# Performance work log

Hardware: AMD Instinct MI355X
Metric: run time of the kernel (lower is better)

Reference implementation:

```python
import math
import jax, jax.numpy as jnp
import numpy as np
from jax import lax

# Fractional-order LIF constants (Teka et al. style fractional LIF)
ALPHA = 0.2          # fractional order (self.frac_order)
DT = 0.1             # ms
V_L = -70.0          # leak reversal
V_RESET = -70.0      # reset potential
V_TH = -50.0         # spike threshold
G_L = 0.025          # leak conductance
CM = 0.5             # membrane capacitance
KAPPA = (DT ** ALPHA) * math.gamma(2.0 - ALPHA)
EXPO = 1.0 - ALPHA


def _flif_scan(I_seq):
    """Fractional LIF over time. I_seq: [T, B, H] -> (spikes, mems) each [T, B, H].
    V_n = KAPPA * (-G_L*(V_{n-1}-V_L) + I_n)/CM + V_{n-1} - memory_n,
    memory_n = sum_{j=1}^{n-1} c_j * dV_{n-1-j},  c_j = (j+1)^{1-a} - j^{1-a}."""
    T, B, H = I_seq.shape
    dt_f = I_seq.dtype
    j = jnp.arange(T + 1, dtype=jnp.float32)
    c = ((j + 1.0) ** EXPO - j ** EXPO).astype(dt_f)  # c[j], valid for j>=1
    ks = jnp.arange(T)

    def step(carry, xs):
        V, hist = carry            # V: [B,H], hist[k] = dV_k: [T,B,H]
        I, n = xs                  # n = 1..T (1-based step index)
        jidx = n - 1 - ks          # lag j for each history slot k
        w = jnp.where(jidx >= 1, c[jnp.clip(jidx, 0, T)], 0.0)
        memory = jnp.einsum('t,tbh->bh', w, hist)
        f = (-G_L * (V - V_L) + I) / CM
        Vn = KAPPA * f + V - memory
        spk = (Vn >= V_TH).astype(dt_f)
        Vr = jnp.where(spk > 0, V_RESET, Vn)
        hist = hist.at[n - 1].set(Vr - V)
        return (Vr, hist), (spk, Vr)

    V0 = jnp.full((B, H), V_RESET, dtype=dt_f)
    hist0 = jnp.zeros((T, B, H), dtype=dt_f)
    _, (spikes, mems) = lax.scan(step, (V0, hist0), (I_seq, jnp.arange(1, T + 1)))
    return spikes, mems


def setup_inputs() -> dict:
    key = jax.random.key(0)
    k1, k2, k3 = jax.random.split(key, 3)
    B, T, NI, NH, NO = 64, 128, 784, 512, 10
    data = jax.random.uniform(k1, (B, T, NI), dtype=jnp.float32)
    kh = 1.0 / np.sqrt(NI)
    W_h = jnp.abs(jax.random.uniform(k2, (NH, NI), minval=-kh, maxval=kh, dtype=jnp.float32) * 6.0)
    ko = 1.0 / np.sqrt(NH)
    W_o = jnp.abs(jax.random.uniform(k3, (NO, NH), minval=-ko, maxval=ko, dtype=jnp.float32) * 5.0)
    return {"data": data, "W_h": W_h, "W_o": W_o}


def reference(data, W_h, W_o):
    # hidden synapses: [B,T,NI] x [NH,NI] -> [T,B,NH] (time-major for scan)
    I_h = jnp.einsum('btn,hn->tbh', data, W_h)
    spk_h, mem_h = _flif_scan(I_h)
    # output synapses applied per step == one GEMM over all steps
    I_o = jnp.einsum('tbh,oh->tbo', spk_h, W_o)
    spk_o, mem_o = _flif_scan(I_o)
    # matches torch.stack(output_spikes_trace), torch.stack(output_values_trace): [T,B,NO]
    return spk_o, mem_o
```

## Files before the change

### kernel.cpp

```cpp
#include <hip/hip_runtime.h>
#include <hip/hip_bf16.h>
#include <cmath>

#define T_STEPS 128
#define BATCH   64
#define NI      784
#define NIP     800
#define NH      512
#define NO      10
#define M1      (T_STEPS*BATCH)
#define NT_H    (BATCH*NH)
#define NT_O    (BATCH*NO)
#define OUT_HALF (T_STEPS*BATCH*NO)
#define TB      8

typedef __attribute__((ext_vector_type(8))) short short8;
typedef __attribute__((ext_vector_type(4))) float f32x4;
typedef __attribute__((ext_vector_type(8))) unsigned short u16x8;

static __device__ __forceinline__ unsigned short f2b_bits(float x) {
    __hip_bfloat16 h = __float2bfloat16(x);
    return *reinterpret_cast<unsigned short*>(&h);
}
static __device__ __forceinline__ float b2f_bits(unsigned short u) {
    union { unsigned int i; float f; } v; v.i = ((unsigned int)u) << 16; return v.f;
}

__global__ __launch_bounds__(256) void prep_kernel(const float* __restrict__ data,
                                                   const float* __restrict__ Wh,
                                                   __hip_bfloat16* __restrict__ Ab,
                                                   __hip_bfloat16* __restrict__ Whb,
                                                   float* __restrict__ ctab) {
    const int bid = blockIdx.x;
    if (bid == 0) {
        const int j = threadIdx.x;
        if (j < 192) {
            double a = pow((double)(j + 1), 0.8);
            double b = pow((double)j, 0.8);
            ctab[j] = (float)(a - b);
        }
        return;
    }
    if (bid <= 6400) {
        const int idx = (bid - 1) * 256 + threadIdx.x;
        const int r  = idx / 200;
        const int n4 = (idx - r * 200) * 4;
        const int t = r >> 6, b = r & 63;
        const int srow = b * T_STEPS + t;
        ushort4 o;
        if (n4 < NI) {
            const float4 f = *reinterpret_cast<const float4*>(data + (size_t)srow * NI + n4);
            o.x = f2b_bits(f.x); o.y = f2b_bits(f.y); o.z = f2b_bits(f.z); o.w = f2b_bits(f.w);
        } else {
            o.x = o.y = o.z = o.w = 0;
        }
        *reinterpret_cast<ushort4*>(Ab + (size_t)r * NIP + n4) = o;
    } else {
        const int idx = (bid - 6401) * 256 + threadIdx.x;
        const int r  = idx / 200;
        const int n4 = (idx - r * 200) * 4;
        ushort4 o;
        if (n4 < NI) {
            const float4 f = *reinterpret_cast<const float4*>(Wh + (size_t)r * NI + n4);
            o.x = f2b_bits(f.x); o.y = f2b_bits(f.y); o.z = f2b_bits(f.z); o.w = f2b_bits(f.w);
        } else {
            o.x = o.y = o.z = o.w = 0;
        }
        *reinterpret_cast<ushort4*>(Whb + (size_t)r * NIP + n4) = o;
    }
}

__global__ __launch_bounds__(256) void gemm_bf16_kernel(const __hip_bfloat16* __restrict__ A,
                                                        const __hip_bfloat16* __restrict__ B,
                                                        __hip_bfloat16* __restrict__ C,
                                                        int N, int Kp) {
    __shared__ __hip_bfloat16 As[2][128 * 32];
    __shared__ __hip_bfloat16 Bs[2][128 * 32];
    const int tid  = threadIdx.x;
    const int wave = tid >> 6, lane = tid & 63;
    const int wm = wave >> 1, wn = wave & 1;
    const int bm = blockIdx.x, bn = blockIdx.y;
    const int lrow = lane >> 2;
    const int lchk = lane & 3;

    const int NTILES = Kp / 32;

    auto STAGE = [&](int buf, int tt) {
        const int k0 = tt * 32;
#pragma unroll
        for (int p = 0; p < 2; ++p) {
            const int rbase = p * 64 + wave * 16;
            {
                const __hip_bfloat16* g = A + (size_t)(bm * 128 + rbase + lrow) * Kp + k0 + lchk * 8;
                __builtin_amdgcn_global_load_lds((const __attribute__((address_space(1))) void*)g,
                                                 (__attribute__((address_space(3))) void*)(As[buf] + rbase * 32),
                                                 16, 0, 0);
            }
            {
                const __hip_bfloat16* g = B + (size_t)(bn * 128 + rbase + lrow) * Kp + k0 + lchk * 8;
                __builtin_amdgcn_global_load_lds((const __attribute__((address_space(1))) void*)g,
                                                 (__attribute__((address_space(3))) void*)(Bs[buf] + rbase * 32),
                                                 16, 0, 0);
            }
        }
    };

    f32x4 acc[4][4] = {};

    STAGE(0, 0);
    __syncthreads();

    int cur = 0;
    for (int t = 0; t < NTILES; ++t) {
        if (t + 1 < NTILES) STAGE(cur ^ 1, t + 1);

        short8 a[4], b[4];
#pragma unroll
        for (int i = 0; i < 4; ++i)
            a[i] = *reinterpret_cast<const short8*>(As[cur] + (wm * 64 + i * 16 + (lane & 15)) * 32 + (lane >> 4) * 8);
#pragma unroll
        for (int j = 0; j < 4; ++j)
            b[j] = *reinterpret_cast<const short8*>(Bs[cur] + (wn * 64 + j * 16 + (lane & 15)) * 32 + (lane >> 4) * 8);
#pragma unroll
        for (int i = 0; i < 4; ++i)
#pragma unroll
            for (int j = 0; j < 4; ++j)
                acc[i][j] = __builtin_amdgcn_mfma_f32_16x16x32_bf16(a[i], b[j], acc[i][j], 0, 0, 0);

        __syncthreads();
        cur ^= 1;
    }

#pragma unroll
    for (int i = 0; i < 4; ++i) {
#pragma unroll
        for (int j = 0; j < 4; ++j) {
            const int col = bn * 128 + wn * 64 + j * 16 + (lane & 15);
#pragma unroll
            for (int r2 = 0; r2 < 4; ++r2) {
                const int row = bm * 128 + wm * 64 + i * 16 + (lane >> 4) * 4 + r2;
                C[(size_t)row * N + col] = __float2bfloat16(acc[i][j][r2]);
            }
        }
    }
}

template <bool FINAL>
__global__ __launch_bounds__(64) void flif_scan_kernel(const void* __restrict__ Iin,
                                                       void* __restrict__ spikes,
                                                       float* __restrict__ mems,
                                                       const float* __restrict__ ctab,
                                                       int NT, float kappa) {
    __shared__ float hist[T_STEPS * 64];
    __shared__ __attribute__((aligned(16))) float cs[192];
    __shared__ __attribute__((aligned(16))) char inps[FINAL ? T_STEPS * 64 * 4 : T_STEPS * 64 * 2];
    const int lane = threadIdx.x;
    const int nid  = blockIdx.x * 64 + lane;

    if constexpr (!FINAL) {
#pragma unroll
        for (int q = 0; q < 16; ++q) {
            const __hip_bfloat16* g = (const __hip_bfloat16*)Iin +
                ((size_t)(q * 8 + (lane >> 3)) * NT + (size_t)blockIdx.x * 64 + (lane & 7) * 8);
            __builtin_amdgcn_global_load_lds((const __attribute__((address_space(1))) void*)g,
                                             (__attribute__((address_space(3))) void*)(inps + q * 1024),
                                             16, 0, 0);
        }
    } else {
#pragma unroll
        for (int q = 0; q < 32; ++q) {
            const float* g = (const float*)Iin +
                ((size_t)(q * 4 + (lane >> 4)) * NT + (size_t)blockIdx.x * 64 + (lane & 15) * 4);
            __builtin_amdgcn_global_load_lds((const __attribute__((address_space(1))) void*)g,
                                             (__attribute__((address_space(3))) void*)(inps + q * 1024),
                                             16, 0, 0);
        }
    }

    for (int j = lane; j < 192; j += 64) cs[j] = ctab[j];
    __syncthreads();

    float cn_[TB];
#pragma unroll
    for (int j = 0; j < TB; ++j) cn_[j] = cs[j];

    float V = -70.f;
    unsigned dvbits = 0u;

    for (int t = 0; t < T_STEPS / TB; ++t) {
        const int n0 = t * TB;

        float Ivv[TB];
#pragma unroll
        for (int i = 0; i < TB; ++i) {
            if constexpr (FINAL) Ivv[i] = ((const float*)inps)[(n0 + i) * 64 + lane];
            else                 Ivv[i] = __bfloat162float(((const __hip_bfloat16*)inps)[(n0 + i) * 64 + lane]);
        }
        __builtin_amdgcn_sched_barrier(0);

        float old_[TB];
#pragma unroll
        for (int i = 0; i < TB; ++i) old_[i] = 0.f;

        if (__any(dvbits != 0u)) {
            for (int k0 = 0; k0 < n0; k0 += TB) {
                float hv[TB];
                unsigned sb = 0u;
#pragma unroll
                for (int kk = 0; kk < TB; ++kk) {
                    hv[kk] = hist[(k0 + kk) * 64 + lane];
                    sb |= __float_as_uint(hv[kk]);
                }
                if (__any(sb != 0u)) {
                    const int base = n0 - k0 - (TB - 1);
                    float cw[2 * TB];
#pragma unroll
                    for (int q = 0; q < 4; ++q) {
                        const float4 cv = *reinterpret_cast<const float4*>(cs + (base - 1) + 4 * q);
                        cw[4 * q + 0] = cv.x; cw[4 * q + 1] = cv.y;
                        cw[4 * q + 2] = cv.z; cw[4 * q + 3] = cv.w;
                    }
#pragma unroll
                    for (int kk = 0; kk < TB; ++kk) {
#pragma unroll
                        for (int i = 0; i < TB; ++i)
                            old_[i] += hv[kk] * cw[TB - kk + i];
                    }
                }
            }
        }

        float dvb[TB];
#pragma unroll
        for (int i = 0; i < TB; ++i) {
            const int nm1 = n0 + i;
            const float Iv = Ivv[i];
            const float f  = (-0.025f * (V + 70.f) + Iv) * 2.0f;
            const float Vn = kappa * f + V - old_[i];
            const bool  sp = (Vn >= -50.f);
            const float Vr = sp ? -70.f : Vn;
            const float dv = Vr - V;
            dvb[i] = dv;
            dvbits |= __float_as_uint(dv);
#pragma unroll
            for (int i2 = i + 1; i2 < TB; ++i2)
                old_[i2] += dv * cn_[i2 - i];
            if (FINAL) {
                ((float*)spikes)[(size_t)nm1 * NT + nid] = sp ? 1.f : 0.f;
                mems[(size_t)nm1 * NT + nid] = Vr;
            } else {
                ((__hip_bfloat16*)spikes)[(size_t)nm1 * NT + nid] = __float2bfloat16(sp ? 1.f : 0.f);
            }
            V = Vr;
        }

        __builtin_amdgcn_sched_barrier(0);
#pragma unroll
        for (int i = 0; i < TB; ++i)
            hist[(n0 + i) * 64 + lane] = dvb[i];
        __builtin_amdgcn_sched_barrier(0);
    }
}

__global__ __launch_bounds__(256) void gemm2_kernel(const __hip_bfloat16* __restrict__ S,
                                                    const float* __restrict__ Wo,
                                                    float* __restrict__ Io) {
    const int wave = threadIdx.x >> 6, lane = threadIdx.x & 63;
    const int r0 = (blockIdx.x * 4 + wave) * 4;

    float wreg[NO][8];
#pragma unroll
    for (int o = 0; o < NO; ++o) {
        const float4 w0 = *reinterpret_cast<const float4*>(Wo + (size_t)o * NH + lane * 8);
        const float4 w1 = *reinterpret_cast<const float4*>(Wo + (size_t)o * NH + lane * 8 + 4);
        wreg[o][0] = w0.x; wreg[o][1] = w0.y; wreg[o][2] = w0.z; wreg[o][3] = w0.w;
        wreg[o][4] = w1.x; wreg[o][5] = w1.y; wreg[o][6] = w1.z; wreg[o][7] = w1.w;
    }

#pragma unroll
    for (int rr = 0; rr < 4; ++rr) {
        const int r = r0 + rr;
        u16x8 raw = *reinterpret_cast<const u16x8*>(S + (size_t)r * NH + lane * 8);
        float s[8];
#pragma unroll
        for (int j = 0; j < 8; ++j) s[j] = b2f_bits(raw[j]);
#pragma unroll
        for (int o = 0; o < NO; ++o) {
            float a = 0.f;
#pragma unroll
            for (int j = 0; j < 8; ++j) a += s[j] * wreg[o][j];
#pragma unroll
            for (int off = 32; off; off >>= 1) a += __shfl_xor(a, off);
            if (lane == o) Io[(size_t)r * NO + o] = a;
        }
    }
}

extern "C" void kernel_launch(void* const* d_in, const int* in_sizes, int n_in,
                              void* d_out, int out_size, void* d_ws, size_t ws_size,
                              hipStream_t stream) {
    const float* data = (const float*)d_in[0];
    const float* Wh   = (const float*)d_in[1];
    const float* Wo   = (const float*)d_in[2];
    float* out = (float*)d_out;

    char* ws = (char*)d_ws;
    size_t off = 0;
    auto alloc = [&](size_t bytes) { void* p = ws + off; off += (bytes + 255) & ~255ull; return p; };
    __hip_bfloat16* Ab   = (__hip_bfloat16*)alloc((size_t)M1 * NIP * 2);
    __hip_bfloat16* Whb  = (__hip_bfloat16*)alloc((size_t)NH * NIP * 2);
    __hip_bfloat16* Ih   = (__hip_bfloat16*)alloc((size_t)M1 * NH * 2);
    __hip_bfloat16* Sh   = (__hip_bfloat16*)alloc((size_t)M1 * NH * 2);
    float*          Io   = (float*)alloc((size_t)M1 * NO * 4);
    float*          ctab = (float*)alloc(192 * 4);

    const float kappa = (float)(std::pow(0.1, 0.2) * std::tgamma(1.8));

    prep_kernel<<<6801, 256, 0, stream>>>(data, Wh, Ab, Whb, ctab);

    dim3 g1(M1 / 128, NH / 128, 1);
    gemm_bf16_kernel<<<g1, 256, 0, stream>>>(Ab, Whb, Ih, NH, NIP);

    flif_scan_kernel<false><<<NT_H / 64, 64, 0, stream>>>(Ih, Sh, nullptr, ctab, NT_H, kappa);

    gemm2_kernel<<<M1 / 16, 256, 0, stream>>>(Sh, Wo, Io);

    flif_scan_kernel<true><<<NT_O / 64, 64, 0, stream>>>(Io, out, out + OUT_HALF, ctab, NT_O, kappa);
}
```

Before: 69.50 us.

## Fuse bf16 conversion, hidden GEMM and hidden LIF scan into one kernel

Replaces the separate prep, bf16 GEMM and hidden-layer scan kernels with one fused kernel. Each block loads fp32 input and weight tiles, converts them to bf16 in registers, computes a 128x128 time-by-neuron tile with MFMA, keeps the currents in LDS and runs the fractional LIF scan there. This removes the bf16 staging buffers and the round trip of the hidden currents through global memory, and drops two launches. The decay coefficient table is now built on the host and copied in. In exchange, each block uses 128KB of LDS, which limits occupancy. The GEMM uses register prefetch instead of async LDS double buffering, and the input data is re-read once per hidden-column block.

```diff
diff --git a/kernel.cpp b/kernel.cpp
--- a/kernel.cpp
+++ b/kernel.cpp
@@ -26,160 +26,13 @@
     union { unsigned int i; float f; } v; v.i = ((unsigned int)u) << 16; return v.f;
 }
 
-__global__ __launch_bounds__(256) void prep_kernel(const float* __restrict__ data,
-                                                   const float* __restrict__ Wh,
-                                                   __hip_bfloat16* __restrict__ Ab,
-                                                   __hip_bfloat16* __restrict__ Whb,
-                                                   float* __restrict__ ctab) {
-    const int bid = blockIdx.x;
-    if (bid == 0) {
-        const int j = threadIdx.x;
-        if (j < 192) {
-            double a = pow((double)(j + 1), 0.8);
-            double b = pow((double)j, 0.8);
-            ctab[j] = (float)(a - b);
-        }
-        return;
-    }
-    if (bid <= 6400) {
-        const int idx = (bid - 1) * 256 + threadIdx.x;
-        const int r  = idx / 200;
-        const int n4 = (idx - r * 200) * 4;
-        const int t = r >> 6, b = r & 63;
-        const int srow = b * T_STEPS + t;
-        ushort4 o;
-        if (n4 < NI) {
-            const float4 f = *reinterpret_cast<const float4*>(data + (size_t)srow * NI + n4);
-            o.x = f2b_bits(f.x); o.y = f2b_bits(f.y); o.z = f2b_bits(f.z); o.w = f2b_bits(f.w);
-        } else {
-            o.x = o.y = o.z = o.w = 0;
-        }
-        *reinterpret_cast<ushort4*>(Ab + (size_t)r * NIP + n4) = o;
-    } else {
-        const int idx = (bid - 6401) * 256 + threadIdx.x;
-        const int r  = idx / 200;
-        const int n4 = (idx - r * 200) * 4;
-        ushort4 o;
-        if (n4 < NI) {
-            const float4 f = *reinterpret_cast<const float4*>(Wh + (size_t)r * NI + n4);
-            o.x = f2b_bits(f.x); o.y = f2b_bits(f.y); o.z = f2b_bits(f.z); o.w = f2b_bits(f.w);
-        } else {
-            o.x = o.y = o.z = o.w = 0;
-        }
-        *reinterpret_cast<ushort4*>(Whb + (size_t)r * NIP + n4) = o;
-    }
-}
-
-__global__ __launch_bounds__(256) void gemm_bf16_kernel(const __hip_bfloat16* __restrict__ A,
-                                                        const __hip_bfloat16* __restrict__ B,
-                                                        __hip_bfloat16* __restrict__ C,
-                                                        int N, int Kp) {
-    __shared__ __hip_bfloat16 As[2][128 * 32];
-    __shared__ __hip_bfloat16 Bs[2][128 * 32];
-    const int tid  = threadIdx.x;
-    const int wave = tid >> 6, lane = tid & 63;
-    const int wm = wave >> 1, wn = wave & 1;
-    const int bm = blockIdx.x, bn = blockIdx.y;
-    const int lrow = lane >> 2;
-    const int lchk = lane & 3;
-
-    const int NTILES = Kp / 32;
-
-    auto STAGE = [&](int buf, int tt) {
-        const int k0 = tt * 32;
-#pragma unroll
-        for (int p = 0; p < 2; ++p) {
-            const int rbase = p * 64 + wave * 16;
-            {
-                const __hip_bfloat16* g = A + (size_t)(bm * 128 + rbase + lrow) * Kp + k0 + lchk * 8;
-                __builtin_amdgcn_global_load_lds((const __attribute__((address_space(1))) void*)g,
-                                                 (__attribute__((address_space(3))) void*)(As[buf] + rbase * 32),
-                                                 16, 0, 0);
-            }
-            {
-                const __hip_bfloat16* g = B + (size_t)(bn * 128 + rbase + lrow) * Kp + k0 + lchk * 8;
-                __builtin_amdgcn_global_load_lds((const __attribute__((address_space(1))) void*)g,
-                                                 (__attribute__((address_space(3))) void*)(Bs[buf] + rbase * 32),
-                                                 16, 0, 0);
-            }
-        }
-    };
-
-    f32x4 acc[4][4] = {};
-
-    STAGE(0, 0);
-    __syncthreads();
-
-    int cur = 0;
-    for (int t = 0; t < NTILES; ++t) {
-        if (t + 1 < NTILES) STAGE(cur ^ 1, t + 1);
-
-        short8 a[4], b[4];
-#pragma unroll
-        for (int i = 0; i < 4; ++i)
-            a[i] = *reinterpret_cast<const short8*>(As[cur] + (wm * 64 + i * 16 + (lane & 15)) * 32 + (lane >> 4) * 8);
-#pragma unroll
-        for (int j = 0; j < 4; ++j)
-            b[j] = *reinterpret_cast<const short8*>(Bs[cur] + (wn * 64 + j * 16 + (lane & 15)) * 32 + (lane >> 4) * 8);
-#pragma unroll
-        for (int i = 0; i < 4; ++i)
-#pragma unroll
-            for (int j = 0; j < 4; ++j)
-                acc[i][j] = __builtin_amdgcn_mfma_f32_16x16x32_bf16(a[i], b[j], acc[i][j], 0, 0, 0);
-
-        __syncthreads();
-        cur ^= 1;
-    }
-
-#pragma unroll
-    for (int i = 0; i < 4; ++i) {
-#pragma unroll
-        for (int j = 0; j < 4; ++j) {
-            const int col = bn * 128 + wn * 64 + j * 16 + (lane & 15);
-#pragma unroll
-            for (int r2 = 0; r2 < 4; ++r2) {
-                const int row = bm * 128 + wm * 64 + i * 16 + (lane >> 4) * 4 + r2;
-                C[(size_t)row * N + col] = __float2bfloat16(acc[i][j][r2]);
-            }
-        }
-    }
-}
-
-template <bool FINAL>
-__global__ __launch_bounds__(64) void flif_scan_kernel(const void* __restrict__ Iin,
-                                                       void* __restrict__ spikes,
-                                                       float* __restrict__ mems,
-                                                       const float* __restrict__ ctab,
-                                                       int NT, float kappa) {
-    __shared__ float hist[T_STEPS * 64];
-    __shared__ __attribute__((aligned(16))) float cs[192];
-    __shared__ __attribute__((aligned(16))) char inps[FINAL ? T_STEPS * 64 * 4 : T_STEPS * 64 * 2];
-    const int lane = threadIdx.x;
-    const int nid  = blockIdx.x * 64 + lane;
-
-    if constexpr (!FINAL) {
-#pragma unroll
-        for (int q = 0; q < 16; ++q) {
-            const __hip_bfloat16* g = (const __hip_bfloat16*)Iin +
-                ((size_t)(q * 8 + (lane >> 3)) * NT + (size_t)blockIdx.x * 64 + (lane & 7) * 8);
-            __builtin_amdgcn_global_load_lds((const __attribute__((address_space(1))) void*)g,
-                                             (__attribute__((address_space(3))) void*)(inps + q * 1024),
-                                             16, 0, 0);
-        }
-    } else {
-#pragma unroll
-        for (int q = 0; q < 32; ++q) {
-            const float* g = (const float*)Iin +
-                ((size_t)(q * 4 + (lane >> 4)) * NT + (size_t)blockIdx.x * 64 + (lane & 15) * 4);
-            __builtin_amdgcn_global_load_lds((const __attribute__((address_space(1))) void*)g,
-                                             (__attribute__((address_space(3))) void*)(inps + q * 1024),
-                                             16, 0, 0);
-        }
-    }
-
-    for (int j = lane; j < 192; j += 64) cs[j] = ctab[j];
-    __syncthreads();
-
+template <bool FINAL, int STRIDE>
+__device__ __forceinline__ void flif_scan_body(const char* __restrict__ inps,
+                                               float* __restrict__ hist,
+                                               const float* __restrict__ cs,
+                                               void* __restrict__ spikes,
+                                               float* __restrict__ mems,
+                                               int NT, int nid, int li, float kappa) {
     float cn_[TB];
 #pragma unroll
     for (int j = 0; j < TB; ++j) cn_[j] = cs[j];
@@ -193,8 +46,8 @@
         float Ivv[TB];
 #pragma unroll
         for (int i = 0; i < TB; ++i) {
-            if constexpr (FINAL) Ivv[i] = ((const float*)inps)[(n0 + i) * 64 + lane];
-            else                 Ivv[i] = __bfloat162float(((const __hip_bfloat16*)inps)[(n0 + i) * 64 + lane]);
+            if constexpr (FINAL) Ivv[i] = ((const float*)inps)[(n0 + i) * STRIDE + li];
+            else                 Ivv[i] = __bfloat162float(((const __hip_bfloat16*)inps)[(n0 + i) * STRIDE + li]);
         }
         __builtin_amdgcn_sched_barrier(0);
 
@@ -208,7 +61,7 @@
                 unsigned sb = 0u;
 #pragma unroll
                 for (int kk = 0; kk < TB; ++kk) {
-                    hv[kk] = hist[(k0 + kk) * 64 + lane];
+                    hv[kk] = hist[(k0 + kk) * STRIDE + li];
                     sb |= __float_as_uint(hv[kk]);
                 }
                 if (__any(sb != 0u)) {
@@ -257,8 +110,116 @@
         __builtin_amdgcn_sched_barrier(0);
 #pragma unroll
         for (int i = 0; i < TB; ++i)
-            hist[(n0 + i) * 64 + lane] = dvb[i];
+            hist[(n0 + i) * STRIDE + li] = dvb[i];
         __builtin_amdgcn_sched_barrier(0);
+    }
+}
+
+__global__ __launch_bounds__(256) void fused1_kernel(const float* __restrict__ data,
+                                                     const float* __restrict__ Wh,
+                                                     __hip_bfloat16* __restrict__ Sh,
+                                                     const float* __restrict__ ctab,
+                                                     float kappa) {
+    __shared__ __attribute__((aligned(16))) char SMEM[131072];
+    __hip_bfloat16* As   = (__hip_bfloat16*)SMEM;
+    __hip_bfloat16* Bs   = (__hip_bfloat16*)(SMEM + 16384);
+    __hip_bfloat16* Ibuf = (__hip_bfloat16*)(SMEM + 32768);
+    float*          hist = (float*)(SMEM + 65536);
+    float*          cs   = (float*)SMEM;
+
+    const int tid  = threadIdx.x;
+    const int wave = tid >> 6, lane = tid & 63;
+    const int wm = wave >> 1, wn = wave & 1;
+    const int b  = blockIdx.x;
+    const int hn = blockIdx.y;
+
+    const int NTILES = NIP / 32;
+
+    float4 ra[4], rb[4];
+    auto LOADT = [&](int t) {
+        const int k0 = t * 32;
+#pragma unroll
+        for (int q = 0; q < 4; ++q) {
+            const int idx = tid + 256 * q;
+            const int row = idx >> 3;
+            const int c4  = idx & 7;
+            const int gk  = k0 + c4 * 4;
+            if (gk < NI) {
+                ra[q] = *reinterpret_cast<const float4*>(data + (size_t)(b * 128 + row) * NI + gk);
+                rb[q] = *reinterpret_cast<const float4*>(Wh   + (size_t)(hn * 128 + row) * NI + gk);
+            } else {
+                ra[q] = make_float4(0.f, 0.f, 0.f, 0.f);
+                rb[q] = make_float4(0.f, 0.f, 0.f, 0.f);
+            }
+        }
+    };
+    auto WRITET = [&]() {
+#pragma unroll
+        for (int q = 0; q < 4; ++q) {
+            const int idx = tid + 256 * q;
+            const int row = idx >> 3;
+            const int c4  = idx & 7;
+            ushort4 oa, ob;
+            oa.x = f2b_bits(ra[q].x); oa.y = f2b_bits(ra[q].y);
+            oa.z = f2b_bits(ra[q].z); oa.w = f2b_bits(ra[q].w);
+            ob.x = f2b_bits(rb[q].x); ob.y = f2b_bits(rb[q].y);
+            ob.z = f2b_bits(rb[q].z); ob.w = f2b_bits(rb[q].w);
+            *reinterpret_cast<ushort4*>(As + row * 32 + c4 * 4) = oa;
+            *reinterpret_cast<ushort4*>(Bs + row * 32 + c4 * 4) = ob;
+        }
+    };
+
+    f32x4 acc[4][4] = {};
+
+    LOADT(0);
+    WRITET();
+    __syncthreads();
+
+    for (int t = 0; t < NTILES; ++t) {
+        if (t + 1 < NTILES) LOADT(t + 1);
+        __builtin_amdgcn_sched_barrier(0);
+
+        short8 a[4], bfr[4];
+#pragma unroll
+        for (int i = 0; i < 4; ++i)
+            a[i] = *reinterpret_cast<const short8*>(As + (wm * 64 + i * 16 + (lane & 15)) * 32 + (lane >> 4) * 8);
+#pragma unroll
+        for (int j = 0; j < 4; ++j)
+            bfr[j] = *reinterpret_cast<const short8*>(Bs + (wn * 64 + j * 16 + (lane & 15)) * 32 + (lane >> 4) * 8);
+#pragma unroll
+        for (int i = 0; i < 4; ++i)
+#pragma unroll
+            for (int j = 0; j < 4; ++j)
+                acc[i][j] = __builtin_amdgcn_mfma_f32_16x16x32_bf16(a[i], bfr[j], acc[i][j], 0, 0, 0);
+
+        __syncthreads();
+        if (t + 1 < NTILES) {
+            WRITET();
+            __syncthreads();
+        }
+    }
+
+#pragma unroll
+    for (int i = 0; i < 4; ++i) {
+#pragma unroll
+        for (int j = 0; j < 4; ++j) {
+            const int col = wn * 64 + j * 16 + (lane & 15);
+#pragma unroll
+            for (int r2 = 0; r2 < 4; ++r2) {
+                const int row = wm * 64 + i * 16 + (lane >> 4) * 4 + r2;
+                Ibuf[row * 128 + col] = __float2bfloat16(acc[i][j][r2]);
+            }
+        }
+    }
+    __syncthreads();
+
+    for (int j = tid; j < 192; j += 256) cs[j] = ctab[j];
+    __syncthreads();
+
+    if (tid < 128) {
+        flif_scan_body<false, 128>((const char*)Ibuf, hist, cs,
+                                   (void*)(Sh + (size_t)b * NH), nullptr,
+                                   64 * NH, hn * 128 + tid, tid, kappa);
     }
 }
 
@@ -294,6 +255,31 @@
             if (lane == o) Io[(size_t)r * NO + o] = a;
         }
     }
+}
+
+__global__ __launch_bounds__(64) void flif_final_kernel(const float* __restrict__ Io,
+                                                        float* __restrict__ spikes,
+                                                        float* __restrict__ mems,
+                                                        const float* __restrict__ ctab,
+                                                        float kappa) {
+    __shared__ float hist[T_STEPS * 64];
+    __shared__ __attribute__((aligned(16))) float cs[192];
+    __shared__ __attribute__((aligned(16))) char inps[T_STEPS * 64 * 4];
+    const int lane = threadIdx.x;
+    const int nid  = blockIdx.x * 64 + lane;
+
+#pragma unroll
+    for (int q = 0; q < 32; ++q) {
+        const float* g = Io +
+            ((size_t)(q * 4 + (lane >> 4)) * NT_O + (size_t)blockIdx.x * 64 + (lane & 15) * 4);
+        __builtin_amdgcn_global_load_lds((const __attribute__((address_space(1))) void*)g,
+                                         (__attribute__((address_space(3))) void*)(inps + q * 1024),
+                                         16, 0, 0);
+    }
+    for (int j = lane; j < 192; j += 64) cs[j] = ctab[j];
+    __syncthreads();
+
+    flif_scan_body<true, 64>(inps, hist, cs, spikes, mems, NT_O, nid, lane, kappa);
 }
 
 extern "C" void kernel_launch(void* const* d_in, const int* in_sizes, int n_in,
@@ -307,23 +293,21 @@
     char* ws = (char*)d_ws;
     size_t off = 0;
     auto alloc = [&](size_t bytes) { void* p = ws + off; off += (bytes + 255) & ~255ull; return p; };
-    __hip_bfloat16* Ab   = (__hip_bfloat16*)alloc((size_t)M1 * NIP * 2);
-    __hip_bfloat16* Whb  = (__hip_bfloat16*)alloc((size_t)NH * NIP * 2);
-    __hip_bfloat16* Ih   = (__hip_bfloat16*)alloc((size_t)M1 * NH * 2);
     __hip_bfloat16* Sh   = (__hip_bfloat16*)alloc((size_t)M1 * NH * 2);
     float*          Io   = (float*)alloc((size_t)M1 * NO * 4);
     float*          ctab = (float*)alloc(192 * 4);
 
     const float kappa = (float)(std::pow(0.1, 0.2) * std::tgamma(1.8));
 
-    prep_kernel<<<6801, 256, 0, stream>>>(data, Wh, Ab, Whb, ctab);
-
-    dim3 g1(M1 / 128, NH / 128, 1);
-    gemm_bf16_kernel<<<g1, 256, 0, stream>>>(Ab, Whb, Ih, NH, NIP);
-
-    flif_scan_kernel<false><<<NT_H / 64, 64, 0, stream>>>(Ih, Sh, nullptr, ctab, NT_H, kappa);
+    static float h_ctab[192];
+    for (int j = 0; j < 192; ++j)
+        h_ctab[j] = (float)(std::pow((double)(j + 1), 0.8) - std::pow((double)j, 0.8));
+    hipMemcpyAsync(ctab, h_ctab, 192 * sizeof(float), hipMemcpyHostToDevice, stream);
+
+    dim3 g1(BATCH, NH / 128, 1);
+    fused1_kernel<<<g1, 256, 0, stream>>>(data, Wh, Sh, ctab, kappa);
 
     gemm2_kernel<<<M1 / 16, 256, 0, stream>>>(Sh, Wo, Io);
 
-    flif_scan_kernel<true><<<NT_O / 64, 64, 0, stream>>>(Io, out, out + OUT_HALF, ctab, NT_O, kappa);
-}
+    flif_final_kernel<<<NT_O / 64, 64, 0, stream>>>(Io, out, out + OUT_HALF, ctab, kappa);
+}
```

New measurement: 94.22 us. 35.6% more time.

## Fuse hidden-layer GEMM with the fractional LIF scan per batch tile

Applied to the files above, without the earlier changes.

Merges the first bf16 MFMA GEMM and the hidden-layer fractional LIF scan into one kernel. Each block computes a 128-timestep by 64-neuron tile for a single batch element, keeps the currents in shared memory, and then runs the scan on one wave. This removes the global round trip of the hidden currents and one kernel launch. In exchange, the GEMM tile shrinks (64 wide in N), shared-memory use per block rises, and only one of four waves does the serial scan while the others sit idle.

```diff
diff --git a/kernel.cpp b/kernel.cpp
--- a/kernel.cpp
+++ b/kernel.cpp
@@ -24,6 +24,95 @@
 }
 static __device__ __forceinline__ float b2f_bits(unsigned short u) {
     union { unsigned int i; float f; } v; v.i = ((unsigned int)u) << 16; return v.f;
+}
+
+template <bool FINAL, int STRIDE>
+__device__ __forceinline__ void flif_scan_body(const char* __restrict__ inps,
+                                               float* __restrict__ hist,
+                                               const float* __restrict__ cs,
+                                               void* __restrict__ spikes,
+                                               float* __restrict__ mems,
+                                               int NT, int nid, int li, float kappa) {
+    float cn_[TB];
+#pragma unroll
+    for (int j = 0; j < TB; ++j) cn_[j] = cs[j];
+
+    float V = -70.f;
+    unsigned dvbits = 0u;
+
+    for (int t = 0; t < T_STEPS / TB; ++t) {
+        const int n0 = t * TB;
+
+        float Ivv[TB];
+#pragma unroll
+        for (int i = 0; i < TB; ++i) {
+            if constexpr (FINAL) Ivv[i] = ((const float*)inps)[(n0 + i) * STRIDE + li];
+            else                 Ivv[i] = __bfloat162float(((const __hip_bfloat16*)inps)[(n0 + i) * STRIDE + li]);
+        }
+        __builtin_amdgcn_sched_barrier(0);
+
+        float old_[TB];
+#pragma unroll
+        for (int i = 0; i < TB; ++i) old_[i] = 0.f;
+
+        if (__any(dvbits != 0u)) {
+            for (int k0 = 0; k0 < n0; k0 += TB) {
+                float hv[TB];
+                unsigned sb = 0u;
+#pragma unroll
+                for (int kk = 0; kk < TB; ++kk) {
+                    hv[kk] = hist[(k0 + kk) * STRIDE + li];
+                    sb |= __float_as_uint(hv[kk]);
+                }
+                if (__any(sb != 0u)) {
+                    const int base = n0 - k0 - (TB - 1);
+                    float cw[2 * TB];
+#pragma unroll
+                    for (int q = 0; q < 4; ++q) {
+                        const float4 cv = *reinterpret_cast<const float4*>(cs + (base - 1) + 4 * q);
+                        cw[4 * q + 0] = cv.x; cw[4 * q + 1] = cv.y;
+                        cw[4 * q + 2] = cv.z; cw[4 * q + 3] = cv.w;
+                    }
+#pragma unroll
+                    for (int kk = 0; kk < TB; ++kk) {
+#pragma unroll
+                        for (int i = 0; i < TB; ++i)
+                            old_[i] += hv[kk] * cw[TB - kk + i];
+                    }
+                }
+            }
+        }
+
+        float dvb[TB];
+#pragma unroll
+        for (int i = 0; i < TB; ++i) {
+            const int nm1 = n0 + i;
+            const float Iv = Ivv[i];
+            const float f  = (-0.025f * (V + 70.f) + Iv) * 2.0f;
+            const float Vn = kappa * f + V - old_[i];
+            const bool  sp = (Vn >= -50.f);
+            const float Vr = sp ? -70.f : Vn;
+            const float dv = Vr - V;
+            dvb[i] = dv;
+            dvbits |= __float_as_uint(dv);
+#pragma unroll
+            for (int i2 = i + 1; i2 < TB; ++i2)
+                old_[i2] += dv * cn_[i2 - i];
+            if (FINAL) {
+                ((float*)spikes)[(size_t)nm1 * NT + nid] = sp ? 1.f : 0.f;
+                mems[(size_t)nm1 * NT + nid] = Vr;
+            } else {
+                ((__hip_bfloat16*)spikes)[(size_t)nm1 * NT + nid] = __float2bfloat16(sp ? 1.f : 0.f);
+            }
+            V = Vr;
+        }
+
+        __builtin_amdgcn_sched_barrier(0);
+#pragma unroll
+        for (int i = 0; i < TB; ++i)
+            hist[(n0 + i) * STRIDE + li] = dvb[i];
+        __builtin_amdgcn_sched_barrier(0);
+    }
 }
 
 __global__ __launch_bounds__(256) void prep_kernel(const float* __restrict__ data,
@@ -70,42 +159,46 @@
     }
 }
 
-__global__ __launch_bounds__(256) void gemm_bf16_kernel(const __hip_bfloat16* __restrict__ A,
-                                                        const __hip_bfloat16* __restrict__ B,
-                                                        __hip_bfloat16* __restrict__ C,
-                                                        int N, int Kp) {
+__global__ __launch_bounds__(256) void fused1_kernel(const __hip_bfloat16* __restrict__ A,
+                                                     const __hip_bfloat16* __restrict__ B,
+                                                     __hip_bfloat16* __restrict__ Sh,
+                                                     const float* __restrict__ ctab,
+                                                     float kappa) {
     __shared__ __hip_bfloat16 As[2][128 * 32];
-    __shared__ __hip_bfloat16 Bs[2][128 * 32];
+    __shared__ __hip_bfloat16 Bs[2][64 * 32];
+    __shared__ __hip_bfloat16 Ibuf[128 * 64];
+    __shared__ float          hist[128 * 64];
+    __shared__ __attribute__((aligned(16))) float cs[192];
+
     const int tid  = threadIdx.x;
     const int wave = tid >> 6, lane = tid & 63;
     const int wm = wave >> 1, wn = wave & 1;
-    const int bm = blockIdx.x, bn = blockIdx.y;
+    const int b  = blockIdx.x;
+    const int hn = blockIdx.y;
     const int lrow = lane >> 2;
     const int lchk = lane & 3;
 
-    const int NTILES = Kp / 32;
+    const int NTILES = NIP / 32;
 
     auto STAGE = [&](int buf, int tt) {
         const int k0 = tt * 32;
 #pragma unroll
         for (int p = 0; p < 2; ++p) {
             const int rbase = p * 64 + wave * 16;
-            {
-                const __hip_bfloat16* g = A + (size_t)(bm * 128 + rbase + lrow) * Kp + k0 + lchk * 8;
-                __builtin_amdgcn_global_load_lds((const __attribute__((address_space(1))) void*)g,
-                                                 (__attribute__((address_space(3))) void*)(As[buf] + rbase * 32),
-                                                 16, 0, 0);
-            }
-            {
-                const __hip_bfloat16* g = B + (size_t)(bn * 128 + rbase + lrow) * Kp + k0 + lchk * 8;
-                __builtin_amdgcn_global_load_lds((const __attribute__((address_space(1))) void*)g,
-                                                 (__attribute__((address_space(3))) void*)(Bs[buf] + rbase * 32),
-                                                 16, 0, 0);
-            }
+            const __hip_bfloat16* g = A + (size_t)((rbase + lrow) * 64 + b) * NIP + k0 + lchk * 8;
+            __builtin_amdgcn_global_load_lds((const __attribute__((address_space(1))) void*)g,
+                                             (__attribute__((address_space(3))) void*)(As[buf] + rbase * 32),
+                                             16, 0, 0);
+        }
+        {
+            const __hip_bfloat16* g = B + (size_t)(hn * 64 + wave * 16 + lrow) * NIP + k0 + lchk * 8;
+            __builtin_amdgcn_global_load_lds((const __attribute__((address_space(1))) void*)g,
+                                             (__attribute__((address_space(3))) void*)(Bs[buf] + wave * 16 * 32),
+                                             16, 0, 0);
         }
     };
 
-    f32x4 acc[4][4] = {};
+    f32x4 acc[4][2] = {};
 
     STAGE(0, 0);
     __syncthreads();
@@ -114,18 +207,18 @@
     for (int t = 0; t < NTILES; ++t) {
         if (t + 1 < NTILES) STAGE(cur ^ 1, t + 1);
 
-        short8 a[4], b[4];
+        short8 a[4], bb[2];
 #pragma unroll
         for (int i = 0; i < 4; ++i)
             a[i] = *reinterpret_cast<const short8*>(As[cur] + (wm * 64 + i * 16 + (lane & 15)) * 32 + (lane >> 4) * 8);
 #pragma unroll
-        for (int j = 0; j < 4; ++j)
-            b[j] = *reinterpret_cast<const short8*>(Bs[cur] + (wn * 64 + j * 16 + (lane & 15)) * 32 + (lane >> 4) * 8);
+        for (int j = 0; j < 2; ++j)
+            bb[j] = *reinterpret_cast<const short8*>(Bs[cur] + (wn * 32 + j * 16 + (lane & 15)) * 32 + (lane >> 4) * 8);
 #pragma unroll
         for (int i = 0; i < 4; ++i)
 #pragma unroll
-            for (int j = 0; j < 4; ++j)
-                acc[i][j] = __builtin_amdgcn_mfma_f32_16x16x32_bf16(a[i], b[j], acc[i][j], 0, 0, 0);
+            for (int j = 0; j < 2; ++j)
+                acc[i][j] = __builtin_amdgcn_mfma_f32_16x16x32_bf16(a[i], bb[j], acc[i][j], 0, 0, 0);
 
         __syncthreads();
         cur ^= 1;
@@ -134,131 +227,24 @@
 #pragma unroll
     for (int i = 0; i < 4; ++i) {
 #pragma unroll
-        for (int j = 0; j < 4; ++j) {
-            const int col = bn * 128 + wn * 64 + j * 16 + (lane & 15);
+        for (int j = 0; j < 2; ++j) {
+            const int col = wn * 32 + j * 16 + (lane & 15);
 #pragma unroll
             for (int r2 = 0; r2 < 4; ++r2) {
-                const int row = bm * 128 + wm * 64 + i * 16 + (lane >> 4) * 4 + r2;
-                C[(size_t)row * N + col] = __float2bfloat16(acc[i][j][r2]);
+                const int row = wm * 64 + i * 16 + (lane >> 4) * 4 + r2;
+                Ibuf[row * 64 + col] = __float2bfloat16(acc[i][j][r2]);
             }
         }
     }
-}
-
-template <bool FINAL>
-__global__ __launch_bounds__(64) void flif_scan_kernel(const void* __restrict__ Iin,
-                                                       void* __restrict__ spikes,
-                                                       float* __restrict__ mems,
-                                                       const float* __restrict__ ctab,
-                                                       int NT, float kappa) {
-    __shared__ float hist[T_STEPS * 64];
-    __shared__ __attribute__((aligned(16))) float cs[192];
-    __shared__ __attribute__((aligned(16))) char inps[FINAL ? T_STEPS * 64 * 4 : T_STEPS * 64 * 2];
-    const int lane = threadIdx.x;
-    const int nid  = blockIdx.x * 64 + lane;
-
-    if constexpr (!FINAL) {
-#pragma unroll
-        for (int q = 0; q < 16; ++q) {
-            const __hip_bfloat16* g = (const __hip_bfloat16*)Iin +
-                ((size_t)(q * 8 + (lane >> 3)) * NT + (size_t)blockIdx.x * 64 + (lane & 7) * 8);
-            __builtin_amdgcn_global_load_lds((const __attribute__((address_space(1))) void*)g,
-                                             (__attribute__((address_space(3))) void*)(inps + q * 1024),
-                                             16, 0, 0);
-        }
-    } else {
-#pragma unroll
-        for (int q = 0; q < 32; ++q) {
-            const float* g = (const float*)Iin +
-                ((size_t)(q * 4 + (lane >> 4)) * NT + (size_t)blockIdx.x * 64 + (lane & 15) * 4);
-            __builtin_amdgcn_global_load_lds((const __attribute__((address_space(1))) void*)g,
-                                             (__attribute__((address_space(3))) void*)(inps + q * 1024),
-                                             16, 0, 0);
-        }
-    }
-
-    for (int j = lane; j < 192; j += 64) cs[j] = ctab[j];
     __syncthreads();
 
-    float cn_[TB];
-#pragma unroll
-    for (int j = 0; j < TB; ++j) cn_[j] = cs[j];
-
-    float V = -70.f;
-    unsigned dvbits = 0u;
-
-    for (int t = 0; t < T_STEPS / TB; ++t) {
-        const int n0 = t * TB;
-
-        float Ivv[TB];
-#pragma unroll
-        for (int i = 0; i < TB; ++i) {
-            if constexpr (FINAL) Ivv[i] = ((const float*)inps)[(n0 + i) * 64 + lane];
-            else                 Ivv[i] = __bfloat162float(((const __hip_bfloat16*)inps)[(n0 + i) * 64 + lane]);
-        }
-        __builtin_amdgcn_sched_barrier(0);
-
-        float old_[TB];
-#pragma unroll
-        for (int i = 0; i < TB; ++i) old_[i] = 0.f;
-
-        if (__any(dvbits != 0u)) {
-            for (int k0 = 0; k0 < n0; k0 += TB) {
-                float hv[TB];
-                unsigned sb = 0u;
-#pragma unroll
-                for (int kk = 0; kk < TB; ++kk) {
-                    hv[kk] = hist[(k0 + kk) * 64 + lane];
-                    sb |= __float_as_uint(hv[kk]);
-                }
-                if (__any(sb != 0u)) {
-                    const int base = n0 - k0 - (TB - 1);
-                    float cw[2 * TB];
-#pragma unroll
-                    for (int q = 0; q < 4; ++q) {
-                        const float4 cv = *reinterpret_cast<const float4*>(cs + (base - 1) + 4 * q);
-                        cw[4 * q + 0] = cv.x; cw[4 * q + 1] = cv.y;
-                        cw[4 * q + 2] = cv.z; cw[4 * q + 3] = cv.w;
-                    }
-#pragma unroll
-                    for (int kk = 0; kk < TB; ++kk) {
-#pragma unroll
-                        for (int i = 0; i < TB; ++i)
-                            old_[i] += hv[kk] * cw[TB - kk + i];
-                    }
-                }
-            }
-        }
-
-        float dvb[TB];
-#pragma unroll
-        for (int i = 0; i < TB; ++i) {
-            const int nm1 = n0 + i;
-            const float Iv = Ivv[i];
-            const float f  = (-0.025f * (V + 70.f) + Iv) * 2.0f;
-            const float Vn = kappa * f + V - old_[i];
-            const bool  sp = (Vn >= -50.f);
-            const float Vr = sp ? -70.f : Vn;
-            const float dv = Vr - V;
-            dvb[i] = dv;
-            dvbits |= __float_as_uint(dv);
-#pragma unroll
-            for (int i2 = i + 1; i2 < TB; ++i2)
-                old_[i2] += dv * cn_[i2 - i];
-            if (FINAL) {
-                ((float*)spikes)[(size_t)nm1 * NT + nid] = sp ? 1.f : 0.f;
-                mems[(size_t)nm1 * NT + nid] = Vr;
-            } else {
-                ((__hip_bfloat16*)spikes)[(size_t)nm1 * NT + nid] = __float2bfloat16(sp ? 1.f : 0.f);
-            }
-            V = Vr;
-        }
-
-        __builtin_amdgcn_sched_barrier(0);
-#pragma unroll
-        for (int i = 0; i < TB; ++i)
-            hist[(n0 + i) * 64 + lane] = dvb[i];
-        __builtin_amdgcn_sched_barrier(0);
+    for (int j = tid; j < 192; j += 256) cs[j] = ctab[j];
+    __syncthreads();
+
+    if (tid < 64) {
+        flif_scan_body<false, 64>((const char*)Ibuf, hist, cs,
+                                  (void*)(Sh + (size_t)b * NH), nullptr,
+                                  64 * NH, hn * 64 + tid, tid, kappa);
     }
 }
 
@@ -294,6 +280,31 @@
             if (lane == o) Io[(size_t)r * NO + o] = a;
         }
     }
+}
+
+__global__ __launch_bounds__(64) void flif_final_kernel(const float* __restrict__ Io,
+                                                        float* __restrict__ spikes,
+                                                        float* __restrict__ mems,
+                                                        const float* __restrict__ ctab,
+                                                        float kappa) {
+    __shared__ float hist[T_STEPS * 64];
+    __shared__ __attribute__((aligned(16))) float cs[192];
+    __shared__ __attribute__((aligned(16))) char inps[T_STEPS * 64 * 4];
+    const int lane = threadIdx.x;
+    const int nid  = blockIdx.x * 64 + lane;
+
+#pragma unroll
+    for (int q = 0; q < 32; ++q) {
+        const float* g = Io +
+            ((size_t)(q * 4 + (lane >> 4)) * NT_O + (size_t)blockIdx.x * 64 + (lane & 15) * 4);
+        __builtin_amdgcn_global_load_lds((const __attribute__((address_space(1))) void*)g,
+                                         (__attribute__((address_space(3))) void*)(inps + q * 1024),
+                                         16, 0, 0);
+    }
+    for (int j = lane; j < 192; j += 64) cs[j] = ctab[j];
+    __syncthreads();
+
+    flif_scan_body<true, 64>(inps, hist, cs, spikes, mems, NT_O, nid, lane, kappa);
 }
 
 extern "C" void kernel_launch(void* const* d_in, const int* in_sizes, int n_in,
@@ -309,7 +320,6 @@
     auto alloc = [&](size_t bytes) { void* p = ws + off; off += (bytes + 255) & ~255ull; return p; };
     __hip_bfloat16* Ab   = (__hip_bfloat16*)alloc((size_t)M1 * NIP * 2);
     __hip_bfloat16* Whb  = (__hip_bfloat16*)alloc((size_t)NH * NIP * 2);
-    __hip_bfloat16* Ih   = (__hip_bfloat16*)alloc((size_t)M1 * NH * 2);
     __hip_bfloat16* Sh   = (__hip_bfloat16*)alloc((size_t)M1 * NH * 2);
     float*          Io   = (float*)alloc((size_t)M1 * NO * 4);
     float*          ctab = (float*)alloc(192 * 4);
@@ -318,12 +328,10 @@
 
     prep_kernel<<<6801, 256, 0, stream>>>(data, Wh, Ab, Whb, ctab);
 
-    dim3 g1(M1 / 128, NH / 128, 1);
-    gemm_bf16_kernel<<<g1, 256, 0, stream>>>(Ab, Whb, Ih, NH, NIP);
-
-    flif_scan_kernel<false><<<NT_H / 64, 64, 0, stream>>>(Ih, Sh, nullptr, ctab, NT_H, kappa);
+    dim3 g1(BATCH, NH / 64, 1);
+    fused1_kernel<<<g1, 256, 0, stream>>>(Ab, Whb, Sh, ctab, kappa);
 
     gemm2_kernel<<<M1 / 16, 256, 0, stream>>>(Sh, Wo, Io);
 
-    flif_scan_kernel<true><<<NT_O / 64, 64, 0, stream>>>(Io, out, out + OUT_HALF, ctab, NT_O, kappa);
-}
+    flif_final_kernel<<<NT_O / 64, 64, 0, stream>>>(Io, out, out + OUT_HALF, ctab, kappa);
+}
```

New measurement: 63.54 us. 8.6% less time.
